# Optimization experiments

Measured on AMD Instinct MI355X. Metric: run time of the kernel, lower is better.

Reference implementation:

```python
import jax, jax.numpy as jnp
import numpy as np

E = 1152        # hidden_size
I = 4304        # intermediate_size
H = 16          # num_attention_heads
HD = E // H     # head_dim = 72
EPS = 1e-6
NEG = float(np.finfo(np.float32).min)


def setup_inputs() -> dict:
    key = jax.random.key(0)
    ks = jax.random.split(key, 12)
    B, S = 32, 4096
    sc = 0.02
    return {
        "hidden_state": jax.random.normal(ks[0], (B, S, E), jnp.float32),
        "attention_mask": jnp.ones((B, S), jnp.int32),
        "probe": jax.random.normal(ks[1], (1, 1, E), jnp.float32),
        "in_proj_w": jax.random.normal(ks[2], (3 * E, E), jnp.float32) * sc,
        "in_proj_b": jax.random.normal(ks[3], (3 * E,), jnp.float32) * sc,
        "out_w": jax.random.normal(ks[4], (E, E), jnp.float32) * sc,
        "out_b": jax.random.normal(ks[5], (E,), jnp.float32) * sc,
        "ln_g": jnp.ones((E,), jnp.float32),
        "ln_b": jnp.zeros((E,), jnp.float32),
        "fc1_w": jax.random.normal(ks[6], (I, E), jnp.float32) * sc,
        "fc1_b": jax.random.normal(ks[7], (I,), jnp.float32) * sc,
        "fc2_w": jax.random.normal(ks[8], (E, I), jnp.float32) * sc,
        "fc2_b": jax.random.normal(ks[9], (E,), jnp.float32) * sc,
    }


def _forward(hidden_state, attention_mask, probe, in_proj_w, in_proj_b,
             out_w, out_b, ln_g, ln_b, fc1_w, fc1_b, fc2_w, fc2_b):
    B, S, _ = hidden_state.shape
    wq, wk, wv = jnp.split(in_proj_w, 3, axis=0)   # each [E, E]
    bq, bk, bv = jnp.split(in_proj_b, 3, axis=0)

    # probe query: identical across batch -> compute once. [H, HD]
    q = (probe[0, 0] @ wq.T + bq).reshape(H, HD)
    k = (hidden_state @ wk.T + bk).reshape(B, S, H, HD)
    v = (hidden_state @ wv.T + bv).reshape(B, S, H, HD)

    # additive mask: (1 - mask) * finfo.min, broadcast over heads. [B, S]
    addmask = (1.0 - attention_mask.astype(hidden_state.dtype)) * NEG

    scale = 1.0 / jnp.sqrt(jnp.asarray(HD, hidden_state.dtype))
    scores = jnp.einsum("hd,bshd->bhs", q, k) * scale + addmask[:, None, :]
    attn = jax.nn.softmax(scores, axis=-1)                 # [B, H, S]
    pooled = jnp.einsum("bhs,bshd->bhd", attn, v).reshape(B, E)
    pooled = pooled @ out_w.T + out_b                      # [B, E]

    residual = pooled
    mu = jnp.mean(pooled, axis=-1, keepdims=True)
    var = jnp.mean(jnp.square(pooled - mu), axis=-1, keepdims=True)
    x = (pooled - mu) * jax.lax.rsqrt(var + EPS) * ln_g + ln_b

    h = jax.nn.gelu(x @ fc1_w.T + fc1_b, approximate=True)  # gelu_pytorch_tanh
    mlp_out = h @ fc2_w.T + fc2_b
    return residual + mlp_out                               # [B, E]


def reference(hidden_state, attention_mask, probe, in_proj_w, in_proj_b,
              out_w, out_b, ln_g, ln_b, fc1_w, fc1_b, fc2_w, fc2_b):
    return _forward(hidden_state, attention_mask, probe, in_proj_w, in_proj_b,
                    out_w, out_b, ln_g, ln_b, fc1_w, fc1_b, fc2_w, fc2_b)
```

## Files before the change

kernel.cpp:

```cpp
#include <hip/hip_runtime.h>
#include <math.h>

#define E 1152
#define H 16
#define HD 72
#define B 32
#define S 4096
#define IDIM 4304
#define NSL 16

#define NEGF (-3.402823466e38f)
#define SCALE 0.1178511301977579f

typedef short short8 __attribute__((ext_vector_type(8)));
typedef float f32x4 __attribute__((ext_vector_type(4)));
typedef unsigned int uint4v __attribute__((ext_vector_type(4)));

#define LGKM_BAR() do { asm volatile("s_waitcnt lgkmcnt(0)" ::: "memory"); \
                        __builtin_amdgcn_s_barrier(); } while(0)

__device__ __forceinline__ unsigned int cvtpk_bf16(float lo, float hi){
  unsigned int r;
  asm("v_cvt_pk_bf16_f32 %0, %1, %2" : "=v"(r) : "v"(lo), "v"(hi));
  return r;
}

__device__ __forceinline__ unsigned short f2bf(float x){
  unsigned int u = __float_as_uint(x);
  u = (u + 0x7fffu + ((u >> 16) & 1u)) >> 16;
  return (unsigned short)u;
}

__device__ __forceinline__ int dst_off(int tid, int i){
  int f = tid + 256*i;
  int r = f / 288;
  int c4 = f - r*288;
  return ((r>>2)*72 + (c4>>2))*128 + (r&3)*32 + (c4&3)*8;
}

__device__ __forceinline__ float wredsum(float v){
  v += __shfl_xor(v,32); v += __shfl_xor(v,16); v += __shfl_xor(v,8);
  v += __shfl_xor(v,4);  v += __shfl_xor(v,2);  v += __shfl_xor(v,1);
  return v;
}

__global__ void k_q(const float* __restrict__ probe, const float* __restrict__ ipw,
                    const float* __restrict__ ipb, float* __restrict__ q){
  int tid = threadIdx.x, lane = tid & 63, w = tid >> 6;
  int j = blockIdx.x*4 + w;
  const float2* wr = (const float2*)(ipw + (size_t)j*E);
  const float2* pr = (const float2*)probe;
  float s = 0.f;
  #pragma unroll
  for (int t=0;t<9;++t){
    int e2 = lane + 64*t;
    float2 a = pr[e2], b = wr[e2];
    s = fmaf(a.x, b.x, fmaf(a.y, b.y, s));
  }
  s = wredsum(s);
  if (lane==0) q[j] = s + ipb[j];
}

__global__ void k_qk(const float* __restrict__ q, const float* __restrict__ ipw,
                     const float* __restrict__ ipb, unsigned short* __restrict__ qkfrag,
                     float* __restrict__ cb){
  int idx = blockIdx.x*256 + threadIdx.x;
  int h = idx / E, e = idx % E;
  float s = 0.f;
  #pragma unroll 8
  for (int d=0; d<HD; ++d)
    s = fmaf(q[h*HD+d], ipw[(size_t)(E + h*HD + d)*E + e], s);
  int kk = e >> 5, g = (e >> 3) & 3, j = e & 7;
  qkfrag[(size_t)kk*512 + (g*16 + h)*8 + j] = f2bf(s);
  if (idx < H){
    float c = 0.f;
    for (int d=0; d<HD; ++d) c = fmaf(q[idx*HD+d], ipb[E + idx*HD + d], c);
    cb[idx] = c;
  }
}

__global__ __launch_bounds__(256) void k_fused(
    const float* __restrict__ hidden, const unsigned short* __restrict__ qkfrag,
    const float* __restrict__ cb, const int* __restrict__ mask,
    float* __restrict__ part, float* __restrict__ part_ml){
  __shared__ __attribute__((aligned(16))) char smem[79680];
  float*    D1      = (float*)(smem + 73728);
  float*    f_lds   = (float*)(smem + 78080);
  unsigned* wgtA    = (unsigned*)(smem + 78144);
  float*    mask_lds= (float*)(smem + 78656);

  int tid = threadIdx.x, lane = tid & 63, w = tid >> 6;
  int b = blockIdx.x >> 4, sl = blockIdx.x & 15;
  int s0 = sl * 256;

  mask_lds[tid] = (1.0f - (float)mask[(size_t)b*S + s0 + tid]) * NEGF;

  short8 qkf[9];
  {
    const short8* qf = (const short8*)qkfrag;
    #pragma unroll
    for (int kk=0;kk<9;++kk) qkf[kk] = qf[(9*w + kk)*64 + lane];
  }

  int rA = lane & 15, gA = lane >> 4;
  int aoff = ((rA>>2)*72 + 18*w + (gA>>1))*128 + (rA&3)*32 + (gA&1)*16;
  int g2 = gA & 1;
  int pvb0 = ((2*g2    )*72 + 18*w)*128 + ((lane&15)>>1)*4;
  int pvb1 = ((2*g2 + 1)*72 + 18*w)*128 + ((lane&15)>>1)*4;
  unsigned sel = 0x05040100u + (unsigned)(lane&1)*0x02020202u;
  int h15 = lane & 15;

  f32x4 acc[18];
  #pragma unroll
  for (int c=0;c<18;++c) acc[c] = (f32x4){0.f,0.f,0.f,0.f};

  float m = -INFINITY, lsum = 0.f;
  float scb = SCALE * cb[h15];
  const float* hbase = hidden + ((size_t)b*S + s0)*E;

  {
    const float4* srcp = (const float4*)hbase;
    #pragma unroll
    for (int i=0;i<18;++i){
      float4 v = srcp[tid + 256*i];
      unsigned u0 = cvtpk_bf16(v.x, v.y);
      unsigned u1 = cvtpk_bf16(v.z, v.w);
      *(uint2*)(smem + dst_off(tid, i)) = make_uint2(u0, u1);
    }
  }
  float4 stg0[9];
  {
    const float4* s1 = (const float4*)(hbase + (size_t)18432);
    #pragma unroll
    for (int i=0;i<9;++i) stg0[i] = s1[tid + 256*i];
  }

  for (int st=0; st<16; ++st){
    LGKM_BAR();
    char* tp = (st & 1) ? (smem + 36864) : smem;
    char* tn = (st & 1) ? smem : (smem + 36864);
    const float4* srcp = (const float4*)(hbase + (size_t)(st+1)*18432);

    f32x4 d1 = {0.f,0.f,0.f,0.f};
    #pragma unroll
    for (int kk=0;kk<9;++kk){
      uint4v ub = *(const uint4v*)(tp + aoff + 256*kk);
      d1 = __builtin_amdgcn_mfma_f32_16x16x32_bf16(
             __builtin_bit_cast(short8, ub), qkf[kk], d1, 0, 0, 0);
    }
    #pragma unroll
    for (int q=0;q<4;++q)
      D1[(w*16 + gA*4 + q)*17 + rA] = d1[q];

    LGKM_BAR();

    if (w == 0){
      int hh = lane & 15, gg = lane >> 4;
      float v[4];
      #pragma unroll
      for (int q=0;q<4;++q){
        int R = gg*4 + q;
        float raw = D1[R*17+hh] + D1[(16+R)*17+hh]
                  + D1[(32+R)*17+hh] + D1[(48+R)*17+hh];
        v[q] = fmaf(raw, SCALE, scb) + mask_lds[st*16 + R];
      }
      float sm = fmaxf(fmaxf(v[0],v[1]), fmaxf(v[2],v[3]));
      sm = fmaxf(sm, __shfl_xor(sm,16));
      sm = fmaxf(sm, __shfl_xor(sm,32));
      float f = 1.0f;
      if (__any(sm > m + 8.0f)){
        float mn = fmaxf(m, sm);
        f = __expf(m - mn);
        m = mn; lsum *= f;
      }
      if (lane < 16) f_lds[lane] = f;
      float w0 = __expf(v[0] - m), w1 = __expf(v[1] - m);
      float w2 = __expf(v[2] - m), w3 = __expf(v[3] - m);
      lsum += w0 + w1 + w2 + w3;
      wgtA[(gg*16 + hh)*2    ] = cvtpk_bf16(w0, w1);
      wgtA[(gg*16 + hh)*2 + 1] = cvtpk_bf16(w2, w3);
    }

    LGKM_BAR();

    if (st+1 < 16){
      #pragma unroll
      for (int i=0;i<9;++i){
        unsigned u0 = cvtpk_bf16(stg0[i].x, stg0[i].y);
        unsigned u1 = cvtpk_bf16(stg0[i].z, stg0[i].w);
        *(uint2*)(tn + dst_off(tid, i)) = make_uint2(u0, u1);
      }
    }
    float4 stg1[9];
    if (st+1 < 16){
      #pragma unroll
      for (int i=0;i<9;++i) stg1[i] = srcp[tid + 256*i + 2304];
    }
    __builtin_amdgcn_sched_barrier(0);

    {
      uint4v ua;
      if (gA < 2){
        ua[0] = wgtA[((2*gA  )*16 + h15)*2    ];
        ua[1] = wgtA[((2*gA  )*16 + h15)*2 + 1];
        ua[2] = wgtA[((2*gA+1)*16 + h15)*2    ];
        ua[3] = wgtA[((2*gA+1)*16 + h15)*2 + 1];
      } else {
        ua[0]=0u; ua[1]=0u; ua[2]=0u; ua[3]=0u;
      }
      short8 afrag = __builtin_bit_cast(short8, ua);

      const float4 fv = *(const float4*)(f_lds + gA*4);
      if (fv.x!=1.f || fv.y!=1.f || fv.z!=1.f || fv.w!=1.f){
        #pragma unroll
        for (int c=0;c<18;++c){
          acc[c][0]*=fv.x; acc[c][1]*=fv.y; acc[c][2]*=fv.z; acc[c][3]*=fv.w;
        }
      }
      #pragma unroll
      for (int c=0;c<18;++c){
        const unsigned* p0 = (const unsigned*)(tp + pvb0 + 128*c);
        const unsigned* p1 = (const unsigned*)(tp + pvb1 + 128*c);
        unsigned a0 = p0[0], a1 = p0[8], a2 = p0[16], a3 = p0[24];
        unsigned b0 = p1[0], b1 = p1[8], b2 = p1[16], b3 = p1[24];
        uint4v ub;
        ub[0] = __builtin_amdgcn_perm(a1, a0, sel);
        ub[1] = __builtin_amdgcn_perm(a3, a2, sel);
        ub[2] = __builtin_amdgcn_perm(b1, b0, sel);
        ub[3] = __builtin_amdgcn_perm(b3, b2, sel);
        acc[c] = __builtin_amdgcn_mfma_f32_16x16x32_bf16(
                   afrag, __builtin_bit_cast(short8, ub), acc[c], 0, 0, 0);
      }
    }
    __builtin_amdgcn_sched_barrier(0);

    if (st+1 < 16){
      #pragma unroll
      for (int i=0;i<9;++i){
        unsigned u0 = cvtpk_bf16(stg1[i].x, stg1[i].y);
        unsigned u1 = cvtpk_bf16(stg1[i].z, stg1[i].w);
        *(uint2*)(tn + dst_off(tid, 9+i)) = make_uint2(u0, u1);
      }
    }
    if (st+2 < 16){
      const float4* s2 = (const float4*)(hbase + (size_t)(st+2)*18432);
      #pragma unroll
      for (int i=0;i<9;++i) stg0[i] = s2[tid + 256*i];
    }
  }

  if (w == 0){
    float lt = lsum + __shfl_xor(lsum, 16);
    lt += __shfl_xor(lt, 32);
    if (lane < 16){
      size_t o = ((size_t)(b*NSL + sl)*16 + lane)*2;
      part_ml[o] = m; part_ml[o+1] = lt;
    }
  }
  {
    float* pp = part + ((size_t)(b*NSL + sl))*H*E;
    #pragma unroll
    for (int c=0;c<18;++c){
      int e = 16*(18*w + c) + h15;
      #pragma unroll
      for (int q=0;q<4;++q)
        pp[(size_t)(gA*4 + q)*E + e] = acc[c][q];
    }
  }
}

__global__ void k_ctxred(const float* __restrict__ part, const float* __restrict__ part_ml,
                         float* __restrict__ ctx){
  int idx = blockIdx.x*256 + threadIdx.x;
  int b = idx / (H*E); int he = idx % (H*E); int h = he / E;
  float M = -INFINITY, L = 0.f;
  #pragma unroll 4
  for (int c = 0; c < NSL; ++c){
    size_t o = ((size_t)(b*NSL + c)*16 + h)*2;
    float om = part_ml[o], ol = part_ml[o+1];
    float nm = fmaxf(M, om);
    L = L*__expf(M - nm) + ol*__expf(om - nm);
    M = nm;
  }
  float invL = 1.0f / L;
  float s = 0.f;
  #pragma unroll 4
  for (int sl=0; sl<NSL; ++sl){
    float scl = __expf(part_ml[((size_t)(b*NSL + sl)*16 + h)*2] - M) * invL;
    s = fmaf(part[(size_t)(b*NSL+sl)*H*E + he], scl, s);
  }
  ctx[idx] = s;
}

__global__ __launch_bounds__(256) void k_pool(
    const float* __restrict__ ctx, const float* __restrict__ ipw,
    const float* __restrict__ ipb, float* __restrict__ pooled){
  __shared__ float red[4][32];
  int tid = threadIdx.x, lane = tid & 63, w = tid >> 6;
  int j = blockIdx.x;
  int h = j / HD;
  const float2* wr = (const float2*)(ipw + (size_t)2*E*E + (size_t)j*E);
  float acc[32];
  #pragma unroll
  for (int b_=0;b_<32;++b_) acc[b_]=0.f;
  for (int t=w; t<9; t+=4){
    int e2 = lane + 64*t;
    float2 wv = wr[e2];
    #pragma unroll
    for (int b_=0;b_<32;++b_){
      float2 cv = *(const float2*)(ctx + (size_t)(b_*H + h)*E + 2*e2);
      acc[b_] = fmaf(wv.x, cv.x, fmaf(wv.y, cv.y, acc[b_]));
    }
  }
  #pragma unroll
  for (int b_=0;b_<32;++b_){
    float s = wredsum(acc[b_]);
    if (lane==b_) red[w][b_] = s;
  }
  __syncthreads();
  if (tid < 32){
    float s = red[0][tid] + red[1][tid] + red[2][tid] + red[3][tid];
    pooled[(size_t)tid*E + j] = s + ipb[2*E + j];
  }
}

__global__ __launch_bounds__(256) void k_outproj(
    const float* __restrict__ pooled, const float* __restrict__ ow,
    const float* __restrict__ ob, float* __restrict__ resid){
  __shared__ float red[4][32];
  int tid = threadIdx.x, lane = tid & 63, w = tid >> 6;
  int i = blockIdx.x;
  const float2* wr = (const float2*)(ow + (size_t)i*E);
  float acc[32];
  #pragma unroll
  for (int b_=0;b_<32;++b_) acc[b_]=0.f;
  for (int t=w; t<9; t+=4){
    int e2 = lane + 64*t;
    float2 wv = wr[e2];
    #pragma unroll
    for (int b_=0;b_<32;++b_){
      float2 pv = *(const float2*)(pooled + (size_t)b_*E + 2*e2);
      acc[b_] = fmaf(wv.x, pv.x, fmaf(wv.y, pv.y, acc[b_]));
    }
  }
  #pragma unroll
  for (int b_=0;b_<32;++b_){
    float s = wredsum(acc[b_]);
    if (lane==b_) red[w][b_] = s;
  }
  __syncthreads();
  if (tid < 32){
    float s = red[0][tid] + red[1][tid] + red[2][tid] + red[3][tid];
    resid[(size_t)tid*E + i] = s + ob[i];
  }
}

__global__ void k_ln(const float* __restrict__ resid, const float* __restrict__ g,
                     const float* __restrict__ be, float* __restrict__ x){
  __shared__ float red[8];
  int b = blockIdx.x, tid = threadIdx.x, lane = tid & 63, w = tid >> 6;
  const float* r = resid + (size_t)b*E;
  float s = 0.f, s2 = 0.f;
  for (int e=tid; e<E; e+=256){ float v = r[e]; s += v; s2 = fmaf(v,v,s2); }
  s = wredsum(s); s2 = wredsum(s2);
  if (lane==0){ red[w]=s; red[4+w]=s2; }
  __syncthreads();
  float S1 = red[0]+red[1]+red[2]+red[3];
  float S2 = red[4]+red[5]+red[6]+red[7];
  float mu  = S1*(1.0f/E);
  float var = S2*(1.0f/E) - mu*mu;
  float inv = rsqrtf(var + 1e-6f);
  for (int e=tid; e<E; e+=256){
    float v = (r[e]-mu)*inv;
    x[(size_t)b*E + e] = v*g[e] + be[e];
  }
}

__device__ __forceinline__ float gelu_tanh(float u){
  float u3 = u*u*u;
  float t = tanhf(0.7978845608028654f*(u + 0.044715f*u3));
  return 0.5f*u*(1.0f+t);
}

__global__ __launch_bounds__(256) void k_fc1(
    const float* __restrict__ x, const float* __restrict__ w1,
    const float* __restrict__ b1, float* __restrict__ h1){
  __shared__ float red[4][2][32];
  int tid = threadIdx.x, lane = tid & 63, w = tid >> 6;
  int i0 = blockIdx.x*2;
  float acc[2][32];
  #pragma unroll
  for (int ii=0;ii<2;++ii)
    #pragma unroll
    for (int b_=0;b_<32;++b_) acc[ii][b_]=0.f;
  const float2* w1a = (const float2*)(w1 + (size_t)i0*E);
  const float2* w1b = (const float2*)(w1 + (size_t)(i0+1)*E);
  for (int t=w; t<9; t+=4){
    int e2 = lane + 64*t;
    float2 f0 = w1a[e2];
    float2 f1 = w1b[e2];
    #pragma unroll
    for (int b_=0;b_<32;++b_){
      float2 xv = *(const float2*)(x + (size_t)b_*E + 2*e2);
      acc[0][b_] = fmaf(f0.x, xv.x, fmaf(f0.y, xv.y, acc[0][b_]));
      acc[1][b_] = fmaf(f1.x, xv.x, fmaf(f1.y, xv.y, acc[1][b_]));
    }
  }
  #pragma unroll
  for (int ii=0;ii<2;++ii)
    #pragma unroll
    for (int b_=0;b_<32;++b_){
      float s = wredsum(acc[ii][b_]);
      if (lane==b_) red[w][ii][b_] = s;
    }
  __syncthreads();
  if (tid < 64){
    int b_ = tid & 31, ii = tid >> 5;
    float s = red[0][ii][b_] + red[1][ii][b_] + red[2][ii][b_] + red[3][ii][b_];
    h1[(size_t)b_*IDIM + i0 + ii] = gelu_tanh(s + b1[i0+ii]);
  }
}

__global__ __launch_bounds__(256) void k_fc2(
    const float* __restrict__ h1, const float* __restrict__ w2,
    const float* __restrict__ b2, const float* __restrict__ resid,
    float* __restrict__ out){
  __shared__ float red[4][2][32];
  int tid = threadIdx.x, lane = tid & 63, w = tid >> 6;
  int i0 = blockIdx.x*2;
  float acc[2][32];
  #pragma unroll
  for (int ii=0;ii<2;++ii)
    #pragma unroll
    for (int b_=0;b_<32;++b_) acc[ii][b_]=0.f;
  for (int t=w; t<68; t+=4){
    int e = lane + 64*t;
    if (e < IDIM){
      float f0 = w2[(size_t)i0*IDIM + e];
      float f1 = w2[(size_t)(i0+1)*IDIM + e];
      #pragma unroll
      for (int b_=0;b_<32;++b_){
        float hvv = h1[(size_t)b_*IDIM + e];
        acc[0][b_] = fmaf(f0, hvv, acc[0][b_]);
        acc[1][b_] = fmaf(f1, hvv, acc[1][b_]);
      }
    }
  }
  #pragma unroll
  for (int ii=0;ii<2;++ii)
    #pragma unroll
    for (int b_=0;b_<32;++b_){
      float s = wredsum(acc[ii][b_]);
      if (lane==b_) red[w][ii][b_] = s;
    }
  __syncthreads();
  if (tid < 64){
    int b_ = tid & 31, ii = tid >> 5;
    float s = red[0][ii][b_] + red[1][ii][b_] + red[2][ii][b_] + red[3][ii][b_];
    int i = i0 + ii;
    out[(size_t)b_*E + i] = resid[(size_t)b_*E + i] + s + b2[i];
  }
}

extern "C" void kernel_launch(void* const* d_in, const int* in_sizes, int n_in,
                              void* d_out, int out_size, void* d_ws, size_t ws_size,
                              hipStream_t stream){
  const float* hidden = (const float*)d_in[0];
  const int*   mask   = (const int*)d_in[1];
  const float* probe  = (const float*)d_in[2];
  const float* ipw    = (const float*)d_in[3];
  const float* ipb    = (const float*)d_in[4];
  const float* ow     = (const float*)d_in[5];
  const float* ob     = (const float*)d_in[6];
  const float* ln_g   = (const float*)d_in[7];
  const float* ln_b   = (const float*)d_in[8];
  const float* w1     = (const float*)d_in[9];
  const float* b1     = (const float*)d_in[10];
  const float* w2     = (const float*)d_in[11];
  const float* b2     = (const float*)d_in[12];
  float* out = (float*)d_out;
  float* ws  = (float*)d_ws;

  size_t off = 0;
  float* q  = ws + off; off += E;
  float* cb = ws + off; off += 16;
  unsigned short* qkfrag = (unsigned short*)(ws + off); off += 9216;
  float* part_ml = ws + off; off += 32*NSL*16*2;
  float* part    = ws + off; off += (size_t)B*NSL*H*E;
  float* ctx     = ws + off; off += (size_t)B*H*E;
  float* pooled  = ws + off; off += (size_t)B*E;
  float* resid   = ws + off; off += (size_t)B*E;
  float* x       = ws + off; off += (size_t)B*E;
  float* h1      = ws + off;

  k_q       <<<288, 256, 0, stream>>>(probe, ipw, ipb, q);
  k_qk      <<<72, 256, 0, stream>>>(q, ipw, ipb, qkfrag, cb);
  k_fused   <<<B*NSL, 256, 0, stream>>>(hidden, qkfrag, cb, mask, part, part_ml);
  k_ctxred  <<<2304, 256, 0, stream>>>(part, part_ml, ctx);
  k_pool    <<<1152, 256, 0, stream>>>(ctx, ipw, ipb, pooled);
  k_outproj <<<1152, 256, 0, stream>>>(pooled, ow, ob, resid);
  k_ln      <<<32, 256, 0, stream>>>(resid, ln_g, ln_b, x);
  k_fc1     <<<2152, 256, 0, stream>>>(x, w1, b1, h1);
  k_fc2     <<<576, 256, 0, stream>>>(h1, w2, b2, resid, out);
}
```

Baseline: 308.6 us.

## Warp-specialize fused attention kernel into compute and loader wave groups

Doubles the fused attention block to 512 threads. Waves 0-3 run the QK MFMA and softmax. Waves 4-7 act as dedicated producers that load the next hidden-state tile from global memory, convert it to bf16 and write it into the LDS double buffer. The PV accumulation is split across both wave halves, so each wave holds 9 accumulators instead of 18, which reduces register pressure. The goal is to overlap global loads with MFMA work more cleanly, at the cost of a larger block, an extra barrier per step, and producer waves that sit idle during the QK phase.

After: 445.0 us. 44.2% more time.

```diff
diff --git a/kernel.cpp b/kernel.cpp
--- a/kernel.cpp
+++ b/kernel.cpp
@@ -31,8 +31,7 @@
   return (unsigned short)u;
 }
 
-__device__ __forceinline__ int dst_off(int tid, int i){
-  int f = tid + 256*i;
+__device__ __forceinline__ int dst_off_f(int f){
   int r = f / 288;
   int c4 = f - r*288;
   return ((r>>2)*72 + (c4>>2))*128 + (r&3)*32 + (c4&3)*8;
@@ -79,7 +78,7 @@
   }
 }
 
-__global__ __launch_bounds__(256) void k_fused(
+__global__ __launch_bounds__(512, 4) void k_fused(
     const float* __restrict__ hidden, const unsigned short* __restrict__ qkfrag,
     const float* __restrict__ cb, const int* __restrict__ mask,
     float* __restrict__ part, float* __restrict__ part_ml){
@@ -92,65 +91,86 @@
   int tid = threadIdx.x, lane = tid & 63, w = tid >> 6;
   int b = blockIdx.x >> 4, sl = blockIdx.x & 15;
   int s0 = sl * 256;
-
-  mask_lds[tid] = (1.0f - (float)mask[(size_t)b*S + s0 + tid]) * NEGF;
-
-  short8 qkf[9];
-  {
-    const short8* qf = (const short8*)qkfrag;
-    #pragma unroll
-    for (int kk=0;kk<9;++kk) qkf[kk] = qf[(9*w + kk)*64 + lane];
+  int qt = w & 3, half = w >> 2;
+  int il = tid & 255;
+
+  if (tid < 256)
+    mask_lds[tid] = (1.0f - (float)mask[(size_t)b*S + s0 + tid]) * NEGF;
+
+  uint4v uni0[9], uni1[9];
+  const float* hbase = hidden + ((size_t)b*S + s0)*E;
+
+  if (w < 4){
+    const uint4v* qf = (const uint4v*)qkfrag;
+    #pragma unroll
+    for (int kk=0;kk<9;++kk) uni0[kk] = qf[(9*w + kk)*64 + lane];
   }
 
   int rA = lane & 15, gA = lane >> 4;
-  int aoff = ((rA>>2)*72 + 18*w + (gA>>1))*128 + (rA&3)*32 + (gA&1)*16;
+  int aoff = ((rA>>2)*72 + 18*qt + (gA>>1))*128 + (rA&3)*32 + (gA&1)*16;
   int g2 = gA & 1;
-  int pvb0 = ((2*g2    )*72 + 18*w)*128 + ((lane&15)>>1)*4;
-  int pvb1 = ((2*g2 + 1)*72 + 18*w)*128 + ((lane&15)>>1)*4;
+  int cbase = 18*qt + 9*half;
+  int pvb0 = ((2*g2    )*72 + cbase)*128 + ((lane&15)>>1)*4;
+  int pvb1 = ((2*g2 + 1)*72 + cbase)*128 + ((lane&15)>>1)*4;
   unsigned sel = 0x05040100u + (unsigned)(lane&1)*0x02020202u;
   int h15 = lane & 15;
 
-  f32x4 acc[18];
-  #pragma unroll
-  for (int c=0;c<18;++c) acc[c] = (f32x4){0.f,0.f,0.f,0.f};
+  f32x4 acc[9];
+  #pragma unroll
+  for (int c=0;c<9;++c) acc[c] = (f32x4){0.f,0.f,0.f,0.f};
+
+  {
+    const float4* srcp = (const float4*)hbase;
+    #pragma unroll
+    for (int i=0;i<9;++i){
+      int f = tid + 512*i;
+      float4 v = srcp[f];
+      *(uint2*)(smem + dst_off_f(f)) =
+          make_uint2(cvtpk_bf16(v.x, v.y), cvtpk_bf16(v.z, v.w));
+    }
+  }
+  if (w >= 4){
+    const uint4v* s1 = (const uint4v*)(hbase + (size_t)18432);
+    #pragma unroll
+    for (int i=0;i<9;++i){
+      uni0[i] = s1[il + 256*i];
+      uni1[i] = s1[il + 256*(9+i)];
+    }
+  }
+  __syncthreads();
 
   float m = -INFINITY, lsum = 0.f;
   float scb = SCALE * cb[h15];
-  const float* hbase = hidden + ((size_t)b*S + s0)*E;
-
-  {
-    const float4* srcp = (const float4*)hbase;
-    #pragma unroll
-    for (int i=0;i<18;++i){
-      float4 v = srcp[tid + 256*i];
-      unsigned u0 = cvtpk_bf16(v.x, v.y);
-      unsigned u1 = cvtpk_bf16(v.z, v.w);
-      *(uint2*)(smem + dst_off(tid, i)) = make_uint2(u0, u1);
-    }
-  }
-  float4 stg0[9];
-  {
-    const float4* s1 = (const float4*)(hbase + (size_t)18432);
-    #pragma unroll
-    for (int i=0;i<9;++i) stg0[i] = s1[tid + 256*i];
-  }
 
   for (int st=0; st<16; ++st){
-    LGKM_BAR();
     char* tp = (st & 1) ? (smem + 36864) : smem;
     char* tn = (st & 1) ? smem : (smem + 36864);
-    const float4* srcp = (const float4*)(hbase + (size_t)(st+1)*18432);
-
-    f32x4 d1 = {0.f,0.f,0.f,0.f};
-    #pragma unroll
-    for (int kk=0;kk<9;++kk){
-      uint4v ub = *(const uint4v*)(tp + aoff + 256*kk);
-      d1 = __builtin_amdgcn_mfma_f32_16x16x32_bf16(
-             __builtin_bit_cast(short8, ub), qkf[kk], d1, 0, 0, 0);
-    }
-    #pragma unroll
-    for (int q=0;q<4;++q)
-      D1[(w*16 + gA*4 + q)*17 + rA] = d1[q];
+
+    if (w < 4){
+      f32x4 d1 = {0.f,0.f,0.f,0.f};
+      #pragma unroll
+      for (int kk=0;kk<9;++kk){
+        uint4v ub = *(const uint4v*)(tp + aoff + 256*kk);
+        d1 = __builtin_amdgcn_mfma_f32_16x16x32_bf16(
+               __builtin_bit_cast(short8, ub),
+               __builtin_bit_cast(short8, uni0[kk]), d1, 0, 0, 0);
+      }
+      #pragma unroll
+      for (int q=0;q<4;++q)
+        D1[(w*16 + gA*4 + q)*17 + rA] = d1[q];
+    } else if (st+1 < 16){
+      #pragma unroll
+      for (int i=0;i<9;++i){
+        float4 v = __builtin_bit_cast(float4, uni0[i]);
+        *(uint2*)(tn + dst_off_f(il + 256*i)) =
+            make_uint2(cvtpk_bf16(v.x, v.y), cvtpk_bf16(v.z, v.w));
+      }
+      if (st+2 < 16){
+        const uint4v* s2 = (const uint4v*)(hbase + (size_t)(st+2)*18432);
+        #pragma unroll
+        for (int i=0;i<9;++i) uni0[i] = s2[il + 256*i];
+      }
+    }
 
     LGKM_BAR();
 
@@ -179,24 +199,21 @@
       lsum += w0 + w1 + w2 + w3;
       wgtA[(gg*16 + hh)*2    ] = cvtpk_bf16(w0, w1);
       wgtA[(gg*16 + hh)*2 + 1] = cvtpk_bf16(w2, w3);
+    } else if (w >= 4 && st+1 < 16){
+      #pragma unroll
+      for (int i=0;i<9;++i){
+        float4 v = __builtin_bit_cast(float4, uni1[i]);
+        *(uint2*)(tn + dst_off_f(il + 256*(9+i))) =
+            make_uint2(cvtpk_bf16(v.x, v.y), cvtpk_bf16(v.z, v.w));
+      }
+      if (st+2 < 16){
+        const uint4v* s2 = (const uint4v*)(hbase + (size_t)(st+2)*18432);
+        #pragma unroll
+        for (int i=0;i<9;++i) uni1[i] = s2[il + 256*(9+i)];
+      }
     }
 
     LGKM_BAR();
-
-    if (st+1 < 16){
-      #pragma unroll
-      for (int i=0;i<9;++i){
-        unsigned u0 = cvtpk_bf16(stg0[i].x, stg0[i].y);
-        unsigned u1 = cvtpk_bf16(stg0[i].z, stg0[i].w);
-        *(uint2*)(tn + dst_off(tid, i)) = make_uint2(u0, u1);
-      }
-    }
-    float4 stg1[9];
-    if (st+1 < 16){
-      #pragma unroll
-      for (int i=0;i<9;++i) stg1[i] = srcp[tid + 256*i + 2304];
-    }
-    __builtin_amdgcn_sched_barrier(0);
 
     {
       uint4v ua;
@@ -213,14 +230,14 @@
       const float4 fv = *(const float4*)(f_lds + gA*4);
       if (fv.x!=1.f || fv.y!=1.f || fv.z!=1.f || fv.w!=1.f){
         #pragma unroll
-        for (int c=0;c<18;++c){
+        for (int c=0;c<9;++c){
           acc[c][0]*=fv.x; acc[c][1]*=fv.y; acc[c][2]*=fv.z; acc[c][3]*=fv.w;
         }
       }
       #pragma unroll
-      for (int c=0;c<18;++c){
-        const unsigned* p0 = (const unsigned*)(tp + pvb0 + 128*c);
-        const unsigned* p1 = (const unsigned*)(tp + pvb1 + 128*c);
+      for (int cl=0; cl<9; ++cl){
+        const unsigned* p0 = (const unsigned*)(tp + pvb0 + 128*cl);
+        const unsigned* p1 = (const unsigned*)(tp + pvb1 + 128*cl);
         unsigned a0 = p0[0], a1 = p0[8], a2 = p0[16], a3 = p0[24];
         unsigned b0 = p1[0], b1 = p1[8], b2 = p1[16], b3 = p1[24];
         uint4v ub;
@@ -228,25 +245,12 @@
         ub[1] = __builtin_amdgcn_perm(a3, a2, sel);
         ub[2] = __builtin_amdgcn_perm(b1, b0, sel);
         ub[3] = __builtin_amdgcn_perm(b3, b2, sel);
-        acc[c] = __builtin_amdgcn_mfma_f32_16x16x32_bf16(
-                   afrag, __builtin_bit_cast(short8, ub), acc[c], 0, 0, 0);
-      }
-    }
-    __builtin_amdgcn_sched_barrier(0);
-
-    if (st+1 < 16){
-      #pragma unroll
-      for (int i=0;i<9;++i){
-        unsigned u0 = cvtpk_bf16(stg1[i].x, stg1[i].y);
-        unsigned u1 = cvtpk_bf16(stg1[i].z, stg1[i].w);
-        *(uint2*)(tn + dst_off(tid, 9+i)) = make_uint2(u0, u1);
-      }
-    }
-    if (st+2 < 16){
-      const float4* s2 = (const float4*)(hbase + (size_t)(st+2)*18432);
-      #pragma unroll
-      for (int i=0;i<9;++i) stg0[i] = s2[tid + 256*i];
-    }
+        acc[cl] = __builtin_amdgcn_mfma_f32_16x16x32_bf16(
+                    afrag, __builtin_bit_cast(short8, ub), acc[cl], 0, 0, 0);
+      }
+    }
+
+    LGKM_BAR();
   }
 
   if (w == 0){
@@ -260,11 +264,11 @@
   {
     float* pp = part + ((size_t)(b*NSL + sl))*H*E;
     #pragma unroll
-    for (int c=0;c<18;++c){
-      int e = 16*(18*w + c) + h15;
+    for (int cl=0; cl<9; ++cl){
+      int e = 16*(cbase + cl) + h15;
       #pragma unroll
       for (int q=0;q<4;++q)
-        pp[(size_t)(gA*4 + q)*E + e] = acc[c][q];
+        pp[(size_t)(gA*4 + q)*E + e] = acc[cl][q];
     }
   }
 }
@@ -495,7 +499,7 @@
 
   k_q       <<<288, 256, 0, stream>>>(probe, ipw, ipb, q);
   k_qk      <<<72, 256, 0, stream>>>(q, ipw, ipb, qkfrag, cb);
-  k_fused   <<<B*NSL, 256, 0, stream>>>(hidden, qkfrag, cb, mask, part, part_ml);
+  k_fused   <<<B*NSL, 512, 0, stream>>>(hidden, qkfrag, cb, mask, part, part_ml);
   k_ctxred  <<<2304, 256, 0, stream>>>(part, part_ml, ctx);
   k_pool    <<<1152, 256, 0, stream>>>(ctx, ipw, ipb, pooled);
   k_outproj <<<1152, 256, 0, stream>>>(pooled, ow, ob, resid);
```
